# Kernel optimization log

Hardware: AMD Instinct MI355X
Metric: run time of the kernel (lower is better)

## Reference

```python
import jax, jax.numpy as jnp
import numpy as np

B, N, D = 4, 2048, 256
ALPHA = 0.2  # LeakyReLU negative slope
NEG = -1e9


def setup_inputs() -> dict:
    key = jax.random.key(0)
    ks = jax.random.split(key, 16)
    f = lambda k, s: jax.random.normal(k, s, dtype=jnp.float32)
    sc = 0.02
    spk = jax.random.randint(ks[13], (B, N), 0, 2)
    intra_mask = (spk[:, :, None] == spk[:, None, :]).astype(jnp.int32)
    inter_mask = 1 - intra_mask
    return {
        'inp': f(ks[0], (B, N, D)),
        'emo_vector': f(ks[1], (B, N, D)),
        'event_csk_before': f(ks[2], (B, N, D)),
        'event_csk_after': f(ks[3], (B, N, D)),
        'emo_intra_csk': f(ks[4], (B, N, D)),
        'emo_inter_csk': f(ks[5], (B, N, D)),
        'int_intra_csk': f(ks[6], (B, N, D)),
        'int_inter_csk': f(ks[7], (B, N, D)),
        'W': f(ks[8], (D, D)) * sc,
        'a': f(ks[9], (2 * D,)) * sc,
        'csk_W': f(ks[10], (D, D)) * sc,
        'csk_b': jnp.zeros((D,), jnp.float32),
        'emo_lin_W': f(ks[11], (4, D, D)) * sc,  # order: weight, query, key, value
        'emo_lin_b': jnp.zeros((4, D), jnp.float32),
        'act_lin_W': f(ks[12], (4, D, D)) * sc,
        'act_lin_b': jnp.zeros((4, D), jnp.float32),
        'conv_len': jax.random.randint(ks[14], (B,), N // 2, N + 1),
        'intra_mask': intra_mask,
        'inter_mask': inter_mask,
    }


def _csk_measure(tv, hv, temo, icsk, ocsk, tim, tom, lin_W, lin_b, add_emo):
    # tv/temo: [B,1,D] target vectors; hv: [B,N,D]; tim/tom: [B,1,N] float masks
    wW, qW, kW, vW = lin_W
    wb, qb, kb, vb = lin_b
    q = (tv + temo if add_emo else tv) @ qW + qb            # [B,1,D]
    w_i = icsk @ wW + wb
    w_o = ocsk @ wW + wb
    k_base = hv @ kW + kb
    v_base = hv @ vW + vb
    k_i, v_i = k_base + w_i, v_base + w_i                   # [B,N,D]
    k_o, v_o = k_base + w_o, v_base + w_o
    inv = 1.0 / jnp.sqrt(jnp.float32(D))
    s_i = jnp.einsum('bqd,bnd->bqn', q, k_i) * inv * tim    # [B,1,N]
    s_o = jnp.einsum('bqd,bnd->bqn', q, k_o) * inv * tom
    m = tim + tom
    probs = jax.nn.softmax(jnp.where(m == 0, NEG, s_i + s_o), axis=-1)  # [B,1,N]
    p_i = (probs * tim).transpose(0, 2, 1)                  # [B,N,1]
    p_o = (probs * tom).transpose(0, 2, 1)
    target_enh = p_i * q + p_o * q                          # q broadcasts [B,1,D]->[B,N,D]
    csk_enh = p_i * v_i + p_o * v_o
    return target_enh + csk_enh, probs


def reference(inp, emo_vector, event_csk_before, event_csk_after,
              emo_intra_csk, emo_inter_csk, int_intra_csk, int_inter_csk,
              W, a, csk_W, csk_b, emo_lin_W, emo_lin_b, act_lin_W, act_lin_b,
              conv_len, intra_mask, inter_mask):
    im = intra_mask.astype(jnp.float32)
    om = inter_mask.astype(jnp.float32)
    h = inp @ W                                             # [B,N,D]
    evt = (event_csk_after @ csk_W + csk_b) + (event_csk_before @ csk_W + csk_b)
    # GAT scoring without materializing [B,N,N,2D]:
    # e[b,i,j] = leaky_relu(h[b,i].a1 + (h+evt)[b,j].a2)
    a1, a2 = a[:D], a[D:]
    s1 = h @ a1                                             # [B,N]
    s2 = (h + evt) @ a2                                     # [B,N]
    e_pair = jax.nn.leaky_relu(s1[:, :, None] + s2[:, None, :], ALPHA)  # [B,N,N]
    e = e_pair * im + e_pair * om
    adj = im + om
    attention = jax.nn.softmax(jnp.where(adj == 0, NEG, e), axis=-1)
    h_prime = jnp.einsum('bij,bjd->bid', attention, h)      # [B,N,D]
    # gather target (last utterance) per conversation
    b_idx = jnp.arange(inp.shape[0])
    t_idx = conv_len - 1
    tv = inp[b_idx, t_idx][:, None, :]                      # [B,1,D]
    temo = emo_vector[b_idx, t_idx][:, None, :]
    tim = im[b_idx, t_idx][:, None, :]                      # [B,1,N]
    tom = om[b_idx, t_idx][:, None, :]
    emo_conn, emo_probs = _csk_measure(tv, h_prime, temo, emo_intra_csk,
                                       emo_inter_csk, tim, tom,
                                       emo_lin_W, emo_lin_b, add_emo=True)
    int_conn, act_probs = _csk_measure(tv, h_prime, temo, int_intra_csk,
                                       int_inter_csk, tim, tom,
                                       act_lin_W, act_lin_b, add_emo=False)
    out = h_prime + inp + emo_conn + int_conn
    return jax.nn.relu(out), emo_probs, act_probs
```

## Files before the change

kernel.cpp:

```cpp
#include <hip/hip_runtime.h>
#include <math.h>


namespace {
constexpr int B = 4, N = 2048, D = 256;
constexpr float ALPHA = 0.2f;
constexpr float INVS  = 0.0625f;

constexpr size_t OFF_H     = 0;
constexpr size_t OFF_HP    = 2097152;
constexpr size_t OFF_UE    = 4194304;
constexpr size_t OFF_UA    = 6291456;
constexpr size_t OFF_PPOS  = 8388608;
constexpr size_t OFF_PNEG  = 10486784;
constexpr size_t OFF_S1    = 12584960;
constexpr size_t OFF_S2    = OFF_S1 + 8192;
constexpr size_t OFF_SIDX  = OFF_S2 + 8192;
constexpr size_t OFF_WP    = OFF_SIDX + 8192;
constexpr size_t OFF_WN    = OFF_WP + 8192;
constexpr size_t OFF_PARTP = OFF_WN + 8192;
constexpr size_t OFF_PARTN = OFF_PARTP + 32768;
constexpr size_t OFF_LE    = OFF_PARTN + 32768;
constexpr size_t OFF_LA    = OFF_LE + 8192;
constexpr size_t OFF_SET   = OFF_LA + 8192;
constexpr size_t KQE = OFF_SET + 0;
constexpr size_t WQE = OFF_SET + 1024;
constexpr size_t KQA = OFF_SET + 2048;
constexpr size_t WQA = OFF_SET + 3072;
constexpr size_t QCE = OFF_SET + 4096;
constexpr size_t QCA = OFF_SET + 5120;
constexpr size_t CA2 = OFF_SET + 6144;
constexpr size_t CEc = OFF_SET + 6400;
constexpr size_t CAc = OFF_SET + 6404;
constexpr size_t C2c = OFF_SET + 6408;
constexpr size_t OFF_RNK   = OFF_SET + 8192;
constexpr size_t OFF_C0    = OFF_RNK + 8192;
constexpr size_t OFF_C1    = OFF_C0 + 8192;
constexpr size_t OFF_PARTQ = OFF_C1 + 8192;
constexpr size_t OFF_QE    = OFF_PARTQ + 32768;
constexpr size_t OFF_QA    = OFF_QE + 1024;
constexpr size_t OFF_BT    = OFF_QA + 1024;
constexpr size_t OFF_PCNT  = OFF_BT + 163840;
constexpr size_t OFF_LEU   = OFF_PCNT + 131072;
constexpr size_t OFF_LAU   = OFF_LEU + 8192;
constexpr size_t SMXE      = OFF_LAU + 8192;
constexpr size_t SIVE      = SMXE + 4;
constexpr size_t SMXA      = SIVE + 4;
constexpr size_t SIVA      = SMXA + 4;
}

typedef __attribute__((ext_vector_type(8))) short bf16x8;
typedef __attribute__((ext_vector_type(4))) float f32x4;

__device__ inline float wave_sum(float v) {
#pragma unroll
  for (int off = 32; off > 0; off >>= 1) v += __shfl_xor(v, off, 64);
  return v;
}

__device__ inline ushort f2bf(float x) {
  union { float f; uint u; } v; v.f = x;
  return (ushort)((v.u + 0x7FFFu + ((v.u >> 16) & 1u)) >> 16);
}
__device__ inline uint pk2bf(float a, float b) {
  return (uint)f2bf(a) | ((uint)f2bf(b) << 16);
}
__device__ inline float bf2f(ushort u) {
  union { uint u; float f; } v; v.u = (uint)u << 16;
  return v.f;
}

__global__ __launch_bounds__(256) void k_btq(
    const float* __restrict__ Wm, const float* __restrict__ eW,
    const float* __restrict__ aW, const float* __restrict__ inp,
    const float* __restrict__ emo, const int* __restrict__ cl,
    ushort* __restrict__ bt, float* __restrict__ ws)
{
  __shared__ float smem[64*65];
  if (blockIdx.y < 5) {
    int m = blockIdx.y;
    const float* src = (m == 0) ? Wm : (m == 1) ? eW + 3*65536 : (m == 2) ? eW
                     : (m == 3) ? aW + 3*65536 : aW;
    ushort* dst = bt + (size_t)m*65536;
    int k0 = (blockIdx.x >> 2)*64, n0 = (blockIdx.x & 3)*64;
    int r = threadIdx.x >> 2, c0 = (threadIdx.x & 3)*16;
#pragma unroll
    for (int cc = 0; cc < 16; cc += 4)
      *(float4*)&smem[r*65 + c0+cc] = *(const float4*)&src[(size_t)(k0+r)*256 + n0 + c0 + cc];
    __syncthreads();
    int n = threadIdx.x >> 2, kq = (threadIdx.x & 3)*16;
    uint4 o0, o1;
    o0.x = pk2bf(smem[(kq+ 0)*65+n], smem[(kq+ 1)*65+n]);
    o0.y = pk2bf(smem[(kq+ 2)*65+n], smem[(kq+ 3)*65+n]);
    o0.z = pk2bf(smem[(kq+ 4)*65+n], smem[(kq+ 5)*65+n]);
    o0.w = pk2bf(smem[(kq+ 6)*65+n], smem[(kq+ 7)*65+n]);
    o1.x = pk2bf(smem[(kq+ 8)*65+n], smem[(kq+ 9)*65+n]);
    o1.y = pk2bf(smem[(kq+10)*65+n], smem[(kq+11)*65+n]);
    o1.z = pk2bf(smem[(kq+12)*65+n], smem[(kq+13)*65+n]);
    o1.w = pk2bf(smem[(kq+14)*65+n], smem[(kq+15)*65+n]);
    *(uint4*)&dst[(size_t)(n0+n)*256 + k0 + kq]     = o0;
    *(uint4*)&dst[(size_t)(n0+n)*256 + k0 + kq + 8] = o1;
  } else {
    int c = blockIdx.x;
    int m = blockIdx.y - 5;
    int d = threadIdx.x;
    if (d < 64) {
      int b = d >> 4, kk = d & 15;
      int t = cl[b] - 1;
      size_t idx = ((size_t)b*N + t)*D + c*16 + kk;
      float v = inp[idx];
      if (m == 0) v += emo[idx];
      smem[b*16 + kk] = v;
    }
    __syncthreads();
    const float* Wq = (m ? aW : eW) + (size_t)D*D;
    float acc0 = 0.f, acc1 = 0.f, acc2 = 0.f, acc3 = 0.f;
#pragma unroll
    for (int kk = 0; kk < 16; ++kk) {
      int k = c*16 + kk;
      float w = Wq[(size_t)k*D + d];
      acc0 += smem[0*16+kk]*w; acc1 += smem[1*16+kk]*w;
      acc2 += smem[2*16+kk]*w; acc3 += smem[3*16+kk]*w;
    }
    size_t base = OFF_PARTQ + ((size_t)(m*16 + c)*4)*256 + d;
    ws[base + 0*256] = acc0; ws[base + 1*256] = acc1;
    ws[base + 2*256] = acc2; ws[base + 3*256] = acc3;
  }
}

__global__ __launch_bounds__(256) void k_mgemmh(
    const float* __restrict__ A1, const ushort* __restrict__ bt,
    float* __restrict__ C)
{
  __shared__ ushort As[32*40];
  const int t = threadIdx.x;
  const int lane = t & 63, w = t >> 6;
  const int laneN = lane & 15, kg = lane >> 4;
  const int m0 = blockIdx.x * 32, n0 = blockIdx.y * 128;
  const int srow = t >> 3, sc = (t & 7) * 4;
  f32x4 acc[2][2] = {};
  for (int k0 = 0; k0 < 256; k0 += 32) {
    __syncthreads();
    float4 f = *(const float4*)&A1[(size_t)(m0 + srow)*256 + k0 + sc];
    uint2 o; o.x = pk2bf(f.x, f.y); o.y = pk2bf(f.z, f.w);
    *(uint2*)&As[srow*40 + sc] = o;
    __syncthreads();
    bf16x8 af[2];
#pragma unroll
    for (int i = 0; i < 2; ++i)
      af[i] = *(const bf16x8*)&As[(i*16 + laneN)*40 + kg*8];
#pragma unroll
    for (int j = 0; j < 2; ++j) {
      bf16x8 bf = *(const bf16x8*)&bt[(size_t)(n0 + w*32 + j*16 + laneN)*256 + k0 + kg*8];
#pragma unroll
      for (int i = 0; i < 2; ++i)
        acc[i][j] = __builtin_amdgcn_mfma_f32_16x16x32_bf16(af[i], bf, acc[i][j], 0, 0, 0);
    }
  }
#pragma unroll
  for (int i = 0; i < 2; ++i)
#pragma unroll
    for (int j = 0; j < 2; ++j)
#pragma unroll
      for (int r = 0; r < 4; ++r)
        C[(size_t)(m0 + i*16 + kg*4 + r)*256 + n0 + w*32 + j*16 + laneN] = acc[i][j][r];
}

__global__ __launch_bounds__(256) void k_qfinish(
    const float* __restrict__ eb, const float* __restrict__ ab,
    const float* __restrict__ cskb, const float* __restrict__ a,
    float* __restrict__ ws)
{
  int b = blockIdx.x, m = blockIdx.y, d = threadIdx.x;
  __shared__ float red[D];
  const float* bias = m ? ab : eb;
  float q = bias[D + d];
#pragma unroll
  for (int c = 0; c < 16; ++c)
    q += ws[OFF_PARTQ + ((size_t)(m*16 + c)*4 + b)*256 + d];
  ws[(m ? OFF_QA : OFF_QE) + (size_t)b*D + d] = q;
  ws[(m ? QCA : QCE) + (size_t)b*D + d] = q + bias[3*D + d] + bias[0*D + d];
  red[d] = q * (bias[2*D + d] + bias[0*D + d]);
  __syncthreads();
  for (int s = 128; s > 0; s >>= 1) { if (d < s) red[d] += red[d+s]; __syncthreads(); }
  if (d == 0) ws[(m ? CAc : CEc) + b] = red[0];
  if (m == 1 && b == 0) {
    __syncthreads();
    red[d] = cskb[d] * a[D + d];
    __syncthreads();
    for (int s = 128; s > 0; s >>= 1) { if (d < s) red[d] += red[d+s]; __syncthreads(); }
    if (d == 0) ws[C2c] = 2.0f * red[0];
  }
}

__global__ __launch_bounds__(256) void k_rowdots(
    const float* __restrict__ eW, const float* __restrict__ aW,
    const float* __restrict__ cskW, const float* __restrict__ a,
    float* __restrict__ ws)
{
  int job = blockIdx.y;
  int wid = threadIdx.x >> 6, lane = threadIdx.x & 63;
  int row = blockIdx.x*4 + wid;
  __shared__ float vec[D];
  const float* M; size_t outo;
  if (job < 16) {
    int b = job >> 2, m = (job >> 1) & 1, which = job & 1;
    const float* base = m ? aW : eW;
    M = base + (which ? 0 : (size_t)2*D*D);
    if (threadIdx.x < D)
      vec[threadIdx.x] = ws[(m ? OFF_QA : OFF_QE) + (size_t)b*D + threadIdx.x];
    outo = (which ? (m ? WQA : WQE) : (m ? KQA : KQE)) + (size_t)b*D;
  } else {
    M = cskW;
    if (threadIdx.x < D) vec[threadIdx.x] = a[D + threadIdx.x];
    outo = CA2;
  }
  __syncthreads();
  float4 w = *reinterpret_cast<const float4*>(&M[(size_t)row*D + lane*4]);
  float s = w.x*vec[lane*4] + w.y*vec[lane*4+1] + w.z*vec[lane*4+2] + w.w*vec[lane*4+3];
  s = wave_sum(s);
  if (lane == 0) ws[outo + row] = s;
}

__global__ __launch_bounds__(256) void k_us(
    const float* __restrict__ ei, const float* __restrict__ eo,
    const float* __restrict__ ai, const float* __restrict__ ao,
    const int* __restrict__ cl, const int* __restrict__ intra,
    const float* __restrict__ bef, const float* __restrict__ aft,
    const float* __restrict__ a, float* __restrict__ ws,
    ushort* __restrict__ ueb, ushort* __restrict__ uab)
{
  if (blockIdx.x < 2048) {
    size_t g = (size_t)blockIdx.x*256 + threadIdx.x;
    size_t base = g << 2;
    int b = (int)(base >> 19);
    int n = (int)((base >> 8) & (N - 1));
    int d0 = (int)(base & (D - 1));
    int t = cl[b] - 1;
    float tm = (float)intra[(size_t)b*N*N + (size_t)t*N + n];
    float om = 1.0f - tm;
    float4 vei = *(const float4*)&ei[base];
    float4 veo = *(const float4*)&eo[base];
    float4 vai = *(const float4*)&ai[base];
    float4 vao = *(const float4*)&ao[base];
    float4 ue, ua;
    ue.x = tm*vei.x + om*veo.x; ue.y = tm*vei.y + om*veo.y;
    ue.z = tm*vei.z + om*veo.z; ue.w = tm*vei.w + om*veo.w;
    ua.x = tm*vai.x + om*vao.x; ua.y = tm*vai.y + om*vao.y;
    ua.z = tm*vai.z + om*vao.z; ua.w = tm*vai.w + om*vao.w;
    uint2 pe; pe.x = pk2bf(ue.x, ue.y); pe.y = pk2bf(ue.z, ue.w);
    uint2 pa; pa.x = pk2bf(ua.x, ua.y); pa.y = pk2bf(ua.z, ua.w);
    *(uint2*)&ueb[base] = pe;
    *(uint2*)&uab[base] = pa;
    float4 wqe = *(const float4*)&ws[WQE + (size_t)b*D + d0];
    float4 wqa = *(const float4*)&ws[WQA + (size_t)b*D + d0];
    float se = ue.x*wqe.x + ue.y*wqe.y + ue.z*wqe.z + ue.w*wqe.w;
    float sa = ua.x*wqa.x + ua.y*wqa.y + ua.z*wqa.z + ua.w*wqa.w;
    se = wave_sum(se); sa = wave_sum(sa);
    if ((threadIdx.x & 63) == 0) {
      size_t row = base >> 8;
      ws[OFF_LEU + row] = se;
      ws[OFF_LAU + row] = sa;
    }
  } else {
    int wid  = (int)(((size_t)(blockIdx.x - 2048)*256 + threadIdx.x) >> 6);
    int lane = threadIdx.x & 63;
    int d0 = lane << 2;
    float4 a1 = *(const float4*)&a[d0];
    float4 a2 = *(const float4*)&a[D + d0];
    float4 cv = *(const float4*)&ws[CA2 + d0];
    float c2  = ws[C2c];
    for (int rr = 0; rr < 4; ++rr) {
      int row = wid*4 + rr;
      float4 h4 = *(const float4*)&ws[OFF_H + (size_t)row*D + d0];
      float4 b4 = *(const float4*)&bef[(size_t)row*D + d0];
      float4 f4 = *(const float4*)&aft[(size_t)row*D + d0];
      float s1 = h4.x*a1.x + h4.y*a1.y + h4.z*a1.z + h4.w*a1.w;
      float s2 = h4.x*a2.x + h4.y*a2.y + h4.z*a2.z + h4.w*a2.w
               + (b4.x+f4.x)*cv.x + (b4.y+f4.y)*cv.y
               + (b4.z+f4.z)*cv.z + (b4.w+f4.w)*cv.w;
      s1 = wave_sum(s1); s2 = wave_sum(s2);
      if (lane == 0) { ws[OFF_S1 + row] = s1; ws[OFF_S2 + row] = s2 + c2; }
    }
  }
}

__global__ __launch_bounds__(256) void k_cnt2(float* __restrict__ ws)
{
  int jb = blockIdx.x;
  int kb = blockIdx.y;
  int b  = blockIdx.z;
  int tid = threadIdx.x;
  __shared__ float ck[128];
  if (tid < 32)
    *(float4*)&ck[tid*4] = *(const float4*)&ws[OFF_S2 + (size_t)b*N + kb*128 + tid*4];
  __syncthreads();
  int j = jb*256 + tid;
  float v = ws[OFF_S2 + (size_t)b*N + j];
  int kg = kb*128;
  int cnt = 0;
#pragma unroll
  for (int k = 0; k < 128; k += 16) {
    float4 u0 = *(const float4*)&ck[k];
    float4 u1 = *(const float4*)&ck[k+4];
    float4 u2 = *(const float4*)&ck[k+8];
    float4 u3 = *(const float4*)&ck[k+12];
    cnt += (u0.x < v) || (u0.x == v && (kg+k+ 0) < j);
    cnt += (u0.y < v) || (u0.y == v && (kg+k+ 1) < j);
    cnt += (u0.z < v) || (u0.z == v && (kg+k+ 2) < j);
    cnt += (u0.w < v) || (u0.w == v && (kg+k+ 3) < j);
    cnt += (u1.x < v) || (u1.x == v && (kg+k+ 4) < j);
    cnt += (u1.y < v) || (u1.y == v && (kg+k+ 5) < j);
    cnt += (u1.z < v) || (u1.z == v && (kg+k+ 6) < j);
    cnt += (u1.w < v) || (u1.w == v && (kg+k+ 7) < j);
    cnt += (u2.x < v) || (u2.x == v && (kg+k+ 8) < j);
    cnt += (u2.y < v) || (u2.y == v && (kg+k+ 9) < j);
    cnt += (u2.z < v) || (u2.z == v && (kg+k+10) < j);
    cnt += (u2.w < v) || (u2.w == v && (kg+k+11) < j);
    cnt += (u3.x < v) || (u3.x == v && (kg+k+12) < j);
    cnt += (u3.y < v) || (u3.y == v && (kg+k+13) < j);
    cnt += (u3.z < v) || (u3.z == v && (kg+k+14) < j);
    cnt += (u3.w < v) || (u3.w == v && (kg+k+15) < j);
  }
  ((int*)ws)[OFF_PCNT + ((size_t)(b*16 + kb))*N + j] = cnt;
}

__global__ __launch_bounds__(1024) void k_csr(float* __restrict__ ws)
{
  int b = blockIdx.x, t = threadIdx.x;
  __shared__ float sv[N];
  __shared__ int   sx[N];
  __shared__ float zp[N+1], zn[N+1], tmp[N];
  const int* pc = (const int*)ws + OFF_PCNT;
#pragma unroll
  for (int h = 0; h < 2; ++h) {
    int j = t + h*1024;
    int cnt = 0;
#pragma unroll
    for (int kb = 0; kb < 16; ++kb)
      cnt += pc[((size_t)(b*16 + kb))*N + j];
    float v = ws[OFF_S2 + (size_t)b*N + j];
    sv[cnt] = v; sx[cnt] = j;
  }
  __syncthreads();
#pragma unroll
  for (int h = 0; h < 2; ++h) {
    int r = t + h*1024;
    ((int*)ws)[OFF_SIDX + (size_t)b*N + r] = sx[r];
    float w = expf(sv[r]);
    ws[OFF_WP + (size_t)b*N + r] = w;
    tmp[r] = w;
  }
  __syncthreads();
  for (int off = 1; off < N; off <<= 1) {
    float v0 = (t >= off)        ? tmp[t - off]        : 0.f;
    float v1 = (t + 1024 >= off) ? tmp[t + 1024 - off] : 0.f;
    __syncthreads();
    tmp[t] += v0; tmp[t + 1024] += v1;
    __syncthreads();
  }
  if (t == 0) zp[0] = 0.f;
  zp[t + 1] = tmp[t]; zp[t + 1025] = tmp[t + 1024];
  __syncthreads();
#pragma unroll
  for (int h = 0; h < 2; ++h) {
    int r = t + h*1024;
    float w = expf(ALPHA*sv[r]);
    ws[OFF_WN + (size_t)b*N + r] = w;
    tmp[r] = w;
  }
  __syncthreads();
  for (int off = 1; off < N; off <<= 1) {
    float v0 = (t >= off)        ? tmp[t - off]        : 0.f;
    float v1 = (t + 1024 >= off) ? tmp[t + 1024 - off] : 0.f;
    __syncthreads();
    tmp[t] += v0; tmp[t + 1024] += v1;
    __syncthreads();
  }
  if (t == 0) zn[0] = 0.f;
  zn[t + 1] = tmp[t]; zn[t + 1025] = tmp[t + 1024];
  __syncthreads();
  float zpT = zp[N];
#pragma unroll
  for (int h = 0; h < 2; ++h) {
    int i = t + h*1024;
    float s1i = ws[OFF_S1 + (size_t)b*N + i];
    float th = -s1i;
    int lo = 0, hi = N;
    while (lo < hi) { int mid = (lo + hi) >> 1; if (sv[mid] <= th) lo = mid + 1; else hi = mid; }
    float ep = expf(s1i), en = expf(ALPHA*s1i);
    float den = ep*(zpT - zp[lo]) + en*zn[lo];
    ((int*)ws)[OFF_RNK + (size_t)b*N + i] = lo;
    ws[OFF_C0 + (size_t)b*N + i] = ep/den;
    ws[OFF_C1 + (size_t)b*N + i] = en/den;
  }
}

__global__ __launch_bounds__(256) void k_p1(float* __restrict__ ws)
{
  int c = blockIdx.x, b = blockIdx.y, d = threadIdx.x;
  const int*   sidx = (const int*)ws + OFF_SIDX + (size_t)b*N;
  const float* wp = ws + OFF_WP + (size_t)b*N;
  const float* wn = ws + OFF_WN + (size_t)b*N;
  const float* h  = ws + OFF_H + (size_t)b*N*D;
  float ap = 0.f, an = 0.f;
  for (int r = c*64; r < c*64 + 64; ++r) {
    float hv = h[(size_t)sidx[r]*D + d];
    ap += wp[r]*hv; an += wn[r]*hv;
  }
  ws[OFF_PARTP + ((size_t)b*32 + c)*D + d] = ap;
  ws[OFF_PARTN + ((size_t)b*32 + c)*D + d] = an;
}

__global__ __launch_bounds__(256) void k_p3(float* __restrict__ ws)
{
  int c = blockIdx.x, b = blockIdx.y, d = threadIdx.x;
  const int*   sidx = (const int*)ws + OFF_SIDX + (size_t)b*N;
  const float* wp = ws + OFF_WP + (size_t)b*N;
  const float* wn = ws + OFF_WN + (size_t)b*N;
  const float* h  = ws + OFF_H + (size_t)b*N*D;
  float ap = 0.f, an = 0.f;
  for (int c2 = 0; c2 < c; ++c2) {
    ap += ws[OFF_PARTP + ((size_t)b*32 + c2)*D + d];
    an += ws[OFF_PARTN + ((size_t)b*32 + c2)*D + d];
  }
  for (int r = c*64; r < c*64 + 64; ++r) {
    ws[OFF_PPOS + ((size_t)b*(N+1) + r)*D + d] = ap;
    ws[OFF_PNEG + ((size_t)b*(N+1) + r)*D + d] = an;
    float hv = h[(size_t)sidx[r]*D + d];
    ap += wp[r]*hv; an += wn[r]*hv;
  }
  if (c == 31) {
    ws[OFF_PPOS + ((size_t)b*(N+1) + N)*D + d] = ap;
    ws[OFF_PNEG + ((size_t)b*(N+1) + N)*D + d] = an;
  }
}

__global__ __launch_bounds__(256) void k_hprime2(float* __restrict__ ws,
                                                 ushort* __restrict__ hpb)
{
  int b = blockIdx.y, d = threadIdx.x;
  int i0 = blockIdx.x * 8;
  float totp = ws[OFF_PPOS + ((size_t)b*(N+1) + N)*D + d];
  float kqe = ws[KQE + (size_t)b*D + d];
  float kqa = ws[KQA + (size_t)b*D + d];
  float se[8], sa[8];
#pragma unroll
  for (int ii = 0; ii < 8; ++ii) {
    int i = i0 + ii;
    int   r  = ((const int*)ws)[OFF_RNK + (size_t)b*N + i];
    float c0 = ws[OFF_C0 + (size_t)b*N + i];
    float c1 = ws[OFF_C1 + (size_t)b*N + i];
    float pp = ws[OFF_PPOS + ((size_t)b*(N+1) + r)*D + d];
    float pn = ws[OFF_PNEG + ((size_t)b*(N+1) + r)*D + d];
    float v = c0*(totp - pp) + c1*pn;
    hpb[((size_t)b*N + i)*D + d] = f2bf(v);
    se[ii] = v*kqe;
    sa[ii] = v*kqa;
  }
  __shared__ float lred[16][4];
  int w = d >> 6, lane = d & 63;
#pragma unroll
  for (int ii = 0; ii < 8; ++ii) {
    float s = wave_sum(se[ii]);
    if (lane == 0) lred[ii][w] = s;
    s = wave_sum(sa[ii]);
    if (lane == 0) lred[8 + ii][w] = s;
  }
  __syncthreads();
  if (d < 16) {
    float s = lred[d][0] + lred[d][1] + lred[d][2] + lred[d][3];
    size_t row = (size_t)b*N + i0 + (d & 7);
    if (d < 8) ws[OFF_LE + row] = (s + ws[OFF_LEU + row] + ws[CEc + b]) * INVS;
    else       ws[OFF_LA + row] = (s + ws[OFF_LAU + row] + ws[CAc + b]) * INVS;
  }
}

__global__ __launch_bounds__(256) void k_smred(float* __restrict__ ws)
{
  int b = blockIdx.x, m = blockIdx.y, t = threadIdx.x;
  const float* l = ws + (m ? OFF_LA : OFF_LE) + (size_t)b*N;
  __shared__ float red[256];
  float v[8];
  float mx = -1e30f;
#pragma unroll
  for (int k = 0; k < 8; ++k) { v[k] = l[t*8 + k]; mx = fmaxf(mx, v[k]); }
  red[t] = mx; __syncthreads();
  for (int s = 128; s > 0; s >>= 1) { if (t < s) red[t] = fmaxf(red[t], red[t+s]); __syncthreads(); }
  mx = red[0]; __syncthreads();
  float sum = 0.f;
#pragma unroll
  for (int k = 0; k < 8; ++k) sum += expf(v[k] - mx);
  red[t] = sum; __syncthreads();
  for (int s = 128; s > 0; s >>= 1) { if (t < s) red[t] += red[t+s]; __syncthreads(); }
  if (t == 0) {
    ws[(m ? SMXA : SMXE) + b] = mx;
    ws[(m ? SIVA : SIVE) + b] = 1.0f / red[0];
  }
}

__global__ __launch_bounds__(256) void k_tail(
    const float* __restrict__ inp, const ushort* __restrict__ bt,
    float* __restrict__ ws, float* __restrict__ out,
    const ushort* __restrict__ hpb, const ushort* __restrict__ ueb,
    const ushort* __restrict__ uab)
{
  __shared__ float qec[256], qac[256];
  const int t = threadIdx.x;
  const int m0 = blockIdx.x * 32, n0 = blockIdx.y * 128;
  const int b = m0 >> 11;
  const int lane = t & 63, w = t >> 6;
  const int laneN = lane & 15, kg = lane >> 4;
  qec[t] = ws[QCE + (size_t)b*D + t];
  qac[t] = ws[QCA + (size_t)b*D + t];
  __syncthreads();
  const ushort* Bve = bt + 1*65536;
  const ushort* Bwe = bt + 2*65536;
  const ushort* Bva = bt + 3*65536;
  const ushort* Bwa = bt + 4*65536;
  f32x4 accE[2][2] = {}, accA[2][2] = {};
  for (int k0 = 0; k0 < 256; k0 += 32) {
    bf16x8 bve[2], bwe[2], bva[2], bwa[2];
#pragma unroll
    for (int j = 0; j < 2; ++j) {
      size_t cb = (size_t)(n0 + w*32 + j*16 + laneN)*256 + k0 + kg*8;
      bve[j] = *(const bf16x8*)&Bve[cb];
      bwe[j] = *(const bf16x8*)&Bwe[cb];
      bva[j] = *(const bf16x8*)&Bva[cb];
      bwa[j] = *(const bf16x8*)&Bwa[cb];
    }
#pragma unroll
    for (int i = 0; i < 2; ++i) {
      size_t ab = (size_t)(m0 + i*16 + laneN)*256 + k0 + kg*8;
      bf16x8 hf = *(const bf16x8*)&hpb[ab];
      bf16x8 ef = *(const bf16x8*)&ueb[ab];
      bf16x8 zf = *(const bf16x8*)&uab[ab];
#pragma unroll
      for (int j = 0; j < 2; ++j) {
        accE[i][j] = __builtin_amdgcn_mfma_f32_16x16x32_bf16(hf, bve[j], accE[i][j], 0, 0, 0);
        accE[i][j] = __builtin_amdgcn_mfma_f32_16x16x32_bf16(ef, bwe[j], accE[i][j], 0, 0, 0);
        accA[i][j] = __builtin_amdgcn_mfma_f32_16x16x32_bf16(hf, bva[j], accA[i][j], 0, 0, 0);
        accA[i][j] = __builtin_amdgcn_mfma_f32_16x16x32_bf16(zf, bwa[j], accA[i][j], 0, 0, 0);
      }
    }
  }
  float smxe = ws[SMXE + b], sive = ws[SIVE + b];
  float smxa = ws[SMXA + b], siva = ws[SIVA + b];
  if (blockIdx.y == 0 && t < 32) {
    size_t row = (size_t)m0 + t;
    int n = (int)(row & (N - 1));
    float pe = expf(ws[OFF_LE + row] - smxe) * sive;
    float pa = expf(ws[OFF_LA + row] - smxa) * siva;
    out[(size_t)B*N*D + (size_t)b*N + n] = pe;
    out[(size_t)B*N*D + (size_t)B*N + (size_t)b*N + n] = pa;
  }
#pragma unroll
  for (int i = 0; i < 2; ++i) {
#pragma unroll
    for (int r = 0; r < 4; ++r) {
      size_t row = (size_t)m0 + i*16 + kg*4 + r;
      float pe = expf(ws[OFF_LE + row] - smxe) * sive;
      float pa = expf(ws[OFF_LA + row] - smxa) * siva;
#pragma unroll
      for (int j = 0; j < 2; ++j) {
        int col = n0 + w*32 + j*16 + laneN;
        size_t idx = row*256 + col;
        float hpv = bf2f(hpb[idx]);
        float o = hpv + inp[idx] + pe*(qec[col] + accE[i][j][r]) + pa*(qac[col] + accA[i][j][r]);
        out[idx] = fmaxf(o, 0.f);
      }
    }
  }
}

extern "C" void kernel_launch(void* const* d_in, const int* in_sizes, int n_in,
                              void* d_out, int out_size, void* d_ws, size_t ws_size,
                              hipStream_t stream) {
  const float* inp  = (const float*)d_in[0];
  const float* emo  = (const float*)d_in[1];
  const float* bef  = (const float*)d_in[2];
  const float* aft  = (const float*)d_in[3];
  const float* ei   = (const float*)d_in[4];
  const float* eo   = (const float*)d_in[5];
  const float* ii   = (const float*)d_in[6];
  const float* io   = (const float*)d_in[7];
  const float* W    = (const float*)d_in[8];
  const float* a    = (const float*)d_in[9];
  const float* cskW = (const float*)d_in[10];
  const float* cskb = (const float*)d_in[11];
  const float* eW   = (const float*)d_in[12];
  const float* eb   = (const float*)d_in[13];
  const float* aW   = (const float*)d_in[14];
  const float* ab   = (const float*)d_in[15];
  const int*   cl   = (const int*)d_in[16];
  const int*   intra= (const int*)d_in[17];
  float* ws  = (float*)d_ws;
  float* out = (float*)d_out;
  ushort* bt  = (ushort*)(ws + OFF_BT);
  ushort* hpb = (ushort*)(ws + OFF_HP);
  ushort* ueb = (ushort*)(ws + OFF_UE);
  ushort* uab = (ushort*)(ws + OFF_UA);

  k_btq<<<dim3(16, 7), 256, 0, stream>>>(W, eW, aW, inp, emo, cl, bt, ws);
  k_mgemmh<<<dim3(256, 2), 256, 0, stream>>>(inp, bt, ws + OFF_H);
  k_qfinish<<<dim3(B, 2), 256, 0, stream>>>(eb, ab, cskb, a, ws);
  k_rowdots<<<dim3(64, 17), 256, 0, stream>>>(eW, aW, cskW, a, ws);
  k_us<<<2560, 256, 0, stream>>>(ei, eo, ii, io, cl, intra, bef, aft, a, ws, ueb, uab);
  k_cnt2<<<dim3(8, 16, B), 256, 0, stream>>>(ws);
  k_csr<<<B, 1024, 0, stream>>>(ws);
  k_p1<<<dim3(32, B), 256, 0, stream>>>(ws);
  k_p3<<<dim3(32, B), 256, 0, stream>>>(ws);
  k_hprime2<<<dim3(256, B), 256, 0, stream>>>(ws, hpb);
  k_smred<<<dim3(B, 2), 256, 0, stream>>>(ws);
  k_tail<<<dim3(256, 2), 256, 0, stream>>>(inp, bt, ws, out, hpb, ueb, uab);
}
```

Baseline: 125.2 us.

## Merge prologue kernels and fold softmax reduction into atomics in hprime

Several small launches are folded together. The q-projection is now computed in one pass per (batch, head) block alongside the weight transposes, which removes the partial-sum buffer and the separate qfinish kernel. The h GEMM and the row-dot kernels now share one launch, and the two prefix scans in the CSR kernel run interleaved in a single loop. The softmax max/sum reduction kernel is replaced by atomic accumulation of exp-sums inside hprime, with no max subtraction. That drops a launch but risks overflow and non-deterministic summation order.

```diff
diff --git a/kernel.cpp b/kernel.cpp
--- a/kernel.cpp
+++ b/kernel.cpp
@@ -36,17 +36,14 @@
 constexpr size_t OFF_RNK   = OFF_SET + 8192;
 constexpr size_t OFF_C0    = OFF_RNK + 8192;
 constexpr size_t OFF_C1    = OFF_C0 + 8192;
-constexpr size_t OFF_PARTQ = OFF_C1 + 8192;
-constexpr size_t OFF_QE    = OFF_PARTQ + 32768;
+constexpr size_t OFF_QE    = OFF_C1 + 8192;
 constexpr size_t OFF_QA    = OFF_QE + 1024;
 constexpr size_t OFF_BT    = OFF_QA + 1024;
 constexpr size_t OFF_PCNT  = OFF_BT + 163840;
 constexpr size_t OFF_LEU   = OFF_PCNT + 131072;
 constexpr size_t OFF_LAU   = OFF_LEU + 8192;
-constexpr size_t SMXE      = OFF_LAU + 8192;
-constexpr size_t SIVE      = SMXE + 4;
-constexpr size_t SMXA      = SIVE + 4;
-constexpr size_t SIVA      = SMXA + 4;
+constexpr size_t OFF_SSE   = OFF_LAU + 8192;
+constexpr size_t OFF_SSA   = OFF_SSE + 4;
 }
 
 typedef __attribute__((ext_vector_type(8))) short bf16x8;
@@ -70,19 +67,22 @@
   return v.f;
 }
 
-__global__ __launch_bounds__(256) void k_btq(
+__global__ __launch_bounds__(256) void k_pre(
     const float* __restrict__ Wm, const float* __restrict__ eW,
     const float* __restrict__ aW, const float* __restrict__ inp,
-    const float* __restrict__ emo, const int* __restrict__ cl,
+    const float* __restrict__ emo, const float* __restrict__ eb,
+    const float* __restrict__ ab, const float* __restrict__ cskb,
+    const float* __restrict__ a, const int* __restrict__ cl,
     ushort* __restrict__ bt, float* __restrict__ ws)
 {
   __shared__ float smem[64*65];
-  if (blockIdx.y < 5) {
-    int m = blockIdx.y;
+  int idx = blockIdx.x;
+  if (idx < 80) {
+    int m = idx / 16, bx = idx & 15;
     const float* src = (m == 0) ? Wm : (m == 1) ? eW + 3*65536 : (m == 2) ? eW
                      : (m == 3) ? aW + 3*65536 : aW;
     ushort* dst = bt + (size_t)m*65536;
-    int k0 = (blockIdx.x >> 2)*64, n0 = (blockIdx.x & 3)*64;
+    int k0 = (bx >> 2)*64, n0 = (bx & 3)*64;
     int r = threadIdx.x >> 2, c0 = (threadIdx.x & 3)*16;
 #pragma unroll
     for (int cc = 0; cc < 16; cc += 4)
@@ -101,125 +101,109 @@
     *(uint4*)&dst[(size_t)(n0+n)*256 + k0 + kq]     = o0;
     *(uint4*)&dst[(size_t)(n0+n)*256 + k0 + kq + 8] = o1;
   } else {
-    int c = blockIdx.x;
-    int m = blockIdx.y - 5;
+    int f = idx - 80;
+    int b = f >> 1, m = f & 1;
     int d = threadIdx.x;
-    if (d < 64) {
-      int b = d >> 4, kk = d & 15;
-      int t = cl[b] - 1;
-      size_t idx = ((size_t)b*N + t)*D + c*16 + kk;
-      float v = inp[idx];
-      if (m == 0) v += emo[idx];
-      smem[b*16 + kk] = v;
-    }
+    float* xs  = smem;
+    float* red = smem + 256;
+    int t = cl[b] - 1;
+    float tv = inp[((size_t)b*N + t)*D + d];
+    xs[d] = (m == 0) ? tv + emo[((size_t)b*N + t)*D + d] : tv;
     __syncthreads();
+    const float* bias = m ? ab : eb;
     const float* Wq = (m ? aW : eW) + (size_t)D*D;
-    float acc0 = 0.f, acc1 = 0.f, acc2 = 0.f, acc3 = 0.f;
-#pragma unroll
-    for (int kk = 0; kk < 16; ++kk) {
-      int k = c*16 + kk;
-      float w = Wq[(size_t)k*D + d];
-      acc0 += smem[0*16+kk]*w; acc1 += smem[1*16+kk]*w;
-      acc2 += smem[2*16+kk]*w; acc3 += smem[3*16+kk]*w;
-    }
-    size_t base = OFF_PARTQ + ((size_t)(m*16 + c)*4)*256 + d;
-    ws[base + 0*256] = acc0; ws[base + 1*256] = acc1;
-    ws[base + 2*256] = acc2; ws[base + 3*256] = acc3;
-  }
-}
-
-__global__ __launch_bounds__(256) void k_mgemmh(
-    const float* __restrict__ A1, const ushort* __restrict__ bt,
-    float* __restrict__ C)
-{
-  __shared__ ushort As[32*40];
-  const int t = threadIdx.x;
-  const int lane = t & 63, w = t >> 6;
-  const int laneN = lane & 15, kg = lane >> 4;
-  const int m0 = blockIdx.x * 32, n0 = blockIdx.y * 128;
-  const int srow = t >> 3, sc = (t & 7) * 4;
-  f32x4 acc[2][2] = {};
-  for (int k0 = 0; k0 < 256; k0 += 32) {
-    __syncthreads();
-    float4 f = *(const float4*)&A1[(size_t)(m0 + srow)*256 + k0 + sc];
-    uint2 o; o.x = pk2bf(f.x, f.y); o.y = pk2bf(f.z, f.w);
-    *(uint2*)&As[srow*40 + sc] = o;
-    __syncthreads();
-    bf16x8 af[2];
-#pragma unroll
-    for (int i = 0; i < 2; ++i)
-      af[i] = *(const bf16x8*)&As[(i*16 + laneN)*40 + kg*8];
-#pragma unroll
-    for (int j = 0; j < 2; ++j) {
-      bf16x8 bf = *(const bf16x8*)&bt[(size_t)(n0 + w*32 + j*16 + laneN)*256 + k0 + kg*8];
-#pragma unroll
-      for (int i = 0; i < 2; ++i)
-        acc[i][j] = __builtin_amdgcn_mfma_f32_16x16x32_bf16(af[i], bf, acc[i][j], 0, 0, 0);
-    }
-  }
-#pragma unroll
-  for (int i = 0; i < 2; ++i)
-#pragma unroll
-    for (int j = 0; j < 2; ++j)
-#pragma unroll
-      for (int r = 0; r < 4; ++r)
-        C[(size_t)(m0 + i*16 + kg*4 + r)*256 + n0 + w*32 + j*16 + laneN] = acc[i][j][r];
-}
-
-__global__ __launch_bounds__(256) void k_qfinish(
-    const float* __restrict__ eb, const float* __restrict__ ab,
-    const float* __restrict__ cskb, const float* __restrict__ a,
-    float* __restrict__ ws)
-{
-  int b = blockIdx.x, m = blockIdx.y, d = threadIdx.x;
-  __shared__ float red[D];
-  const float* bias = m ? ab : eb;
-  float q = bias[D + d];
-#pragma unroll
-  for (int c = 0; c < 16; ++c)
-    q += ws[OFF_PARTQ + ((size_t)(m*16 + c)*4 + b)*256 + d];
-  ws[(m ? OFF_QA : OFF_QE) + (size_t)b*D + d] = q;
-  ws[(m ? QCA : QCE) + (size_t)b*D + d] = q + bias[3*D + d] + bias[0*D + d];
-  red[d] = q * (bias[2*D + d] + bias[0*D + d]);
-  __syncthreads();
-  for (int s = 128; s > 0; s >>= 1) { if (d < s) red[d] += red[d+s]; __syncthreads(); }
-  if (d == 0) ws[(m ? CAc : CEc) + b] = red[0];
-  if (m == 1 && b == 0) {
-    __syncthreads();
-    red[d] = cskb[d] * a[D + d];
+    float a0 = 0.f, a1 = 0.f, a2 = 0.f, a3 = 0.f;
+    for (int k = 0; k < 256; k += 4) {
+      a0 += xs[k+0]*Wq[(size_t)(k+0)*256 + d];
+      a1 += xs[k+1]*Wq[(size_t)(k+1)*256 + d];
+      a2 += xs[k+2]*Wq[(size_t)(k+2)*256 + d];
+      a3 += xs[k+3]*Wq[(size_t)(k+3)*256 + d];
+    }
+    float q = bias[D + d] + ((a0 + a1) + (a2 + a3));
+    ws[(m ? OFF_QA : OFF_QE) + (size_t)b*D + d] = q;
+    ws[(m ? QCA : QCE) + (size_t)b*D + d] = q + bias[3*D + d] + bias[0*D + d];
+    red[d] = q * (bias[2*D + d] + bias[0*D + d]);
     __syncthreads();
     for (int s = 128; s > 0; s >>= 1) { if (d < s) red[d] += red[d+s]; __syncthreads(); }
-    if (d == 0) ws[C2c] = 2.0f * red[0];
-  }
-}
-
-__global__ __launch_bounds__(256) void k_rowdots(
+    if (d == 0) ws[(m ? CAc : CEc) + b] = red[0];
+    if (m == 1 && b == 0) {
+      __syncthreads();
+      red[d] = cskb[d] * a[D + d];
+      __syncthreads();
+      for (int s = 128; s > 0; s >>= 1) { if (d < s) red[d] += red[d+s]; __syncthreads(); }
+      if (d == 0) ws[C2c] = 2.0f * red[0];
+    }
+    if (f == 0 && d < 8) ws[OFF_SSE + d] = 0.f;
+  }
+}
+
+__global__ __launch_bounds__(256) void k_hw(
+    const float* __restrict__ inp, const ushort* __restrict__ bt,
     const float* __restrict__ eW, const float* __restrict__ aW,
     const float* __restrict__ cskW, const float* __restrict__ a,
     float* __restrict__ ws)
 {
-  int job = blockIdx.y;
-  int wid = threadIdx.x >> 6, lane = threadIdx.x & 63;
-  int row = blockIdx.x*4 + wid;
-  __shared__ float vec[D];
-  const float* M; size_t outo;
-  if (job < 16) {
-    int b = job >> 2, m = (job >> 1) & 1, which = job & 1;
-    const float* base = m ? aW : eW;
-    M = base + (which ? 0 : (size_t)2*D*D);
-    if (threadIdx.x < D)
-      vec[threadIdx.x] = ws[(m ? OFF_QA : OFF_QE) + (size_t)b*D + threadIdx.x];
-    outo = (which ? (m ? WQA : WQE) : (m ? KQA : KQE)) + (size_t)b*D;
+  __shared__ float smem[640];
+  int idx = blockIdx.x;
+  if (idx < 512) {
+    ushort* As = (ushort*)smem;
+    const int t = threadIdx.x;
+    const int lane = t & 63, w = t >> 6;
+    const int laneN = lane & 15, kg = lane >> 4;
+    const int m0 = (idx >> 1) * 32, n0 = (idx & 1) * 128;
+    const int srow = t >> 3, sc = (t & 7) * 4;
+    float* C = ws + OFF_H;
+    f32x4 acc[2][2] = {};
+    for (int k0 = 0; k0 < 256; k0 += 32) {
+      __syncthreads();
+      float4 f = *(const float4*)&inp[(size_t)(m0 + srow)*256 + k0 + sc];
+      uint2 o; o.x = pk2bf(f.x, f.y); o.y = pk2bf(f.z, f.w);
+      *(uint2*)&As[srow*40 + sc] = o;
+      __syncthreads();
+      bf16x8 af[2];
+#pragma unroll
+      for (int i = 0; i < 2; ++i)
+        af[i] = *(const bf16x8*)&As[(i*16 + laneN)*40 + kg*8];
+#pragma unroll
+      for (int j = 0; j < 2; ++j) {
+        bf16x8 bf = *(const bf16x8*)&bt[(size_t)(n0 + w*32 + j*16 + laneN)*256 + k0 + kg*8];
+#pragma unroll
+        for (int i = 0; i < 2; ++i)
+          acc[i][j] = __builtin_amdgcn_mfma_f32_16x16x32_bf16(af[i], bf, acc[i][j], 0, 0, 0);
+      }
+    }
+#pragma unroll
+    for (int i = 0; i < 2; ++i)
+#pragma unroll
+      for (int j = 0; j < 2; ++j)
+#pragma unroll
+        for (int r = 0; r < 4; ++r)
+          C[(size_t)(m0 + i*16 + kg*4 + r)*256 + n0 + w*32 + j*16 + laneN] = acc[i][j][r];
   } else {
-    M = cskW;
-    if (threadIdx.x < D) vec[threadIdx.x] = a[D + threadIdx.x];
-    outo = CA2;
-  }
-  __syncthreads();
-  float4 w = *reinterpret_cast<const float4*>(&M[(size_t)row*D + lane*4]);
-  float s = w.x*vec[lane*4] + w.y*vec[lane*4+1] + w.z*vec[lane*4+2] + w.w*vec[lane*4+3];
-  s = wave_sum(s);
-  if (lane == 0) ws[outo + row] = s;
+    int f = idx - 512;
+    int job = f >> 6, rb = f & 63;
+    int wid = threadIdx.x >> 6, lane = threadIdx.x & 63;
+    int row = rb*4 + wid;
+    float* vec = smem;
+    const float* M; size_t outo;
+    if (job < 16) {
+      int b = job >> 2, m = (job >> 1) & 1, which = job & 1;
+      const float* base = m ? aW : eW;
+      M = base + (which ? 0 : (size_t)2*D*D);
+      if (threadIdx.x < D)
+        vec[threadIdx.x] = ws[(m ? OFF_QA : OFF_QE) + (size_t)b*D + threadIdx.x];
+      outo = (which ? (m ? WQA : WQE) : (m ? KQA : KQE)) + (size_t)b*D;
+    } else {
+      M = cskW;
+      if (threadIdx.x < D) vec[threadIdx.x] = a[D + threadIdx.x];
+      outo = CA2;
+    }
+    __syncthreads();
+    float4 w = *reinterpret_cast<const float4*>(&M[(size_t)row*D + lane*4]);
+    float s = w.x*vec[lane*4] + w.y*vec[lane*4+1] + w.z*vec[lane*4+2] + w.w*vec[lane*4+3];
+    s = wave_sum(s);
+    if (lane == 0) ws[outo + row] = s;
+  }
 }
 
 __global__ __launch_bounds__(256) void k_us(
@@ -330,7 +314,8 @@
   int b = blockIdx.x, t = threadIdx.x;
   __shared__ float sv[N];
   __shared__ int   sx[N];
-  __shared__ float zp[N+1], zn[N+1], tmp[N];
+  __shared__ float zp[N+1], zn[N+1];
+  __shared__ float tp[N], tn[N];
   const int* pc = (const int*)ws + OFF_PCNT;
 #pragma unroll
   for (int h = 0; h < 2; ++h) {
@@ -347,38 +332,26 @@
   for (int h = 0; h < 2; ++h) {
     int r = t + h*1024;
     ((int*)ws)[OFF_SIDX + (size_t)b*N + r] = sx[r];
-    float w = expf(sv[r]);
-    ws[OFF_WP + (size_t)b*N + r] = w;
-    tmp[r] = w;
+    float wp = expf(sv[r]);
+    float wn = expf(ALPHA*sv[r]);
+    ws[OFF_WP + (size_t)b*N + r] = wp;
+    ws[OFF_WN + (size_t)b*N + r] = wn;
+    tp[r] = wp; tn[r] = wn;
   }
   __syncthreads();
   for (int off = 1; off < N; off <<= 1) {
-    float v0 = (t >= off)        ? tmp[t - off]        : 0.f;
-    float v1 = (t + 1024 >= off) ? tmp[t + 1024 - off] : 0.f;
+    float p0 = (t >= off)        ? tp[t - off]        : 0.f;
+    float n0 = (t >= off)        ? tn[t - off]        : 0.f;
+    float p1 = (t + 1024 >= off) ? tp[t + 1024 - off] : 0.f;
+    float n1 = (t + 1024 >= off) ? tn[t + 1024 - off] : 0.f;
     __syncthreads();
-    tmp[t] += v0; tmp[t + 1024] += v1;
+    tp[t] += p0; tn[t] += n0;
+    tp[t + 1024] += p1; tn[t + 1024] += n1;
     __syncthreads();
   }
-  if (t == 0) zp[0] = 0.f;
-  zp[t + 1] = tmp[t]; zp[t + 1025] = tmp[t + 1024];
-  __syncthreads();
-#pragma unroll
-  for (int h = 0; h < 2; ++h) {
-    int r = t + h*1024;
-    float w = expf(ALPHA*sv[r]);
-    ws[OFF_WN + (size_t)b*N + r] = w;
-    tmp[r] = w;
-  }
-  __syncthreads();
-  for (int off = 1; off < N; off <<= 1) {
-    float v0 = (t >= off)        ? tmp[t - off]        : 0.f;
-    float v1 = (t + 1024 >= off) ? tmp[t + 1024 - off] : 0.f;
-    __syncthreads();
-    tmp[t] += v0; tmp[t + 1024] += v1;
-    __syncthreads();
-  }
-  if (t == 0) zn[0] = 0.f;
-  zn[t + 1] = tmp[t]; zn[t + 1025] = tmp[t + 1024];
+  if (t == 0) { zp[0] = 0.f; zn[0] = 0.f; }
+  zp[t + 1] = tp[t]; zp[t + 1025] = tp[t + 1024];
+  zn[t + 1] = tn[t]; zn[t + 1025] = tn[t + 1024];
   __syncthreads();
   float zpT = zp[N];
 #pragma unroll
@@ -459,6 +432,7 @@
     sa[ii] = v*kqa;
   }
   __shared__ float lred[16][4];
+  __shared__ float l16[16];
   int w = d >> 6, lane = d & 63;
 #pragma unroll
   for (int ii = 0; ii < 8; ++ii) {
@@ -471,31 +445,23 @@
   if (d < 16) {
     float s = lred[d][0] + lred[d][1] + lred[d][2] + lred[d][3];
     size_t row = (size_t)b*N + i0 + (d & 7);
-    if (d < 8) ws[OFF_LE + row] = (s + ws[OFF_LEU + row] + ws[CEc + b]) * INVS;
-    else       ws[OFF_LA + row] = (s + ws[OFF_LAU + row] + ws[CAc + b]) * INVS;
-  }
-}
-
-__global__ __launch_bounds__(256) void k_smred(float* __restrict__ ws)
-{
-  int b = blockIdx.x, m = blockIdx.y, t = threadIdx.x;
-  const float* l = ws + (m ? OFF_LA : OFF_LE) + (size_t)b*N;
-  __shared__ float red[256];
-  float v[8];
-  float mx = -1e30f;
-#pragma unroll
-  for (int k = 0; k < 8; ++k) { v[k] = l[t*8 + k]; mx = fmaxf(mx, v[k]); }
-  red[t] = mx; __syncthreads();
-  for (int s = 128; s > 0; s >>= 1) { if (t < s) red[t] = fmaxf(red[t], red[t+s]); __syncthreads(); }
-  mx = red[0]; __syncthreads();
-  float sum = 0.f;
-#pragma unroll
-  for (int k = 0; k < 8; ++k) sum += expf(v[k] - mx);
-  red[t] = sum; __syncthreads();
-  for (int s = 128; s > 0; s >>= 1) { if (t < s) red[t] += red[t+s]; __syncthreads(); }
-  if (t == 0) {
-    ws[(m ? SMXA : SMXE) + b] = mx;
-    ws[(m ? SIVA : SIVE) + b] = 1.0f / red[0];
+    float lv;
+    if (d < 8) { lv = (s + ws[OFF_LEU + row] + ws[CEc + b]) * INVS; ws[OFF_LE + row] = lv; }
+    else       { lv = (s + ws[OFF_LAU + row] + ws[CAc + b]) * INVS; ws[OFF_LA + row] = lv; }
+    l16[d] = lv;
+  }
+  __syncthreads();
+  if (d == 0) {
+    float s = 0.f;
+#pragma unroll
+    for (int i = 0; i < 8; ++i) s += expf(l16[i]);
+    atomicAdd(&ws[OFF_SSE + b], s);
+  }
+  if (d == 64) {
+    float s = 0.f;
+#pragma unroll
+    for (int i = 8; i < 16; ++i) s += expf(l16[i]);
+    atomicAdd(&ws[OFF_SSA + b], s);
   }
 }
 
@@ -544,13 +510,13 @@
       }
     }
   }
-  float smxe = ws[SMXE + b], sive = ws[SIVE + b];
-  float smxa = ws[SMXA + b], siva = ws[SIVA + b];
+  float sive = 1.0f / ws[OFF_SSE + b];
+  float siva = 1.0f / ws[OFF_SSA + b];
   if (blockIdx.y == 0 && t < 32) {
     size_t row = (size_t)m0 + t;
     int n = (int)(row & (N - 1));
-    float pe = expf(ws[OFF_LE + row] - smxe) * sive;
-    float pa = expf(ws[OFF_LA + row] - smxa) * siva;
+    float pe = expf(ws[OFF_LE + row]) * sive;
+    float pa = expf(ws[OFF_LA + row]) * siva;
     out[(size_t)B*N*D + (size_t)b*N + n] = pe;
     out[(size_t)B*N*D + (size_t)B*N + (size_t)b*N + n] = pa;
   }
@@ -559,8 +525,8 @@
 #pragma unroll
     for (int r = 0; r < 4; ++r) {
       size_t row = (size_t)m0 + i*16 + kg*4 + r;
-      float pe = expf(ws[OFF_LE + row] - smxe) * sive;
-      float pa = expf(ws[OFF_LA + row] - smxa) * siva;
+      float pe = expf(ws[OFF_LE + row]) * sive;
+      float pa = expf(ws[OFF_LA + row]) * siva;
 #pragma unroll
       for (int j = 0; j < 2; ++j) {
         int col = n0 + w*32 + j*16 + laneN;
@@ -601,16 +567,13 @@
   ushort* ueb = (ushort*)(ws + OFF_UE);
   ushort* uab = (ushort*)(ws + OFF_UA);
 
-  k_btq<<<dim3(16, 7), 256, 0, stream>>>(W, eW, aW, inp, emo, cl, bt, ws);
-  k_mgemmh<<<dim3(256, 2), 256, 0, stream>>>(inp, bt, ws + OFF_H);
-  k_qfinish<<<dim3(B, 2), 256, 0, stream>>>(eb, ab, cskb, a, ws);
-  k_rowdots<<<dim3(64, 17), 256, 0, stream>>>(eW, aW, cskW, a, ws);
+  k_pre<<<88, 256, 0, stream>>>(W, eW, aW, inp, emo, eb, ab, cskb, a, cl, bt, ws);
+  k_hw<<<1600, 256, 0, stream>>>(inp, bt, eW, aW, cskW, a, ws);
   k_us<<<2560, 256, 0, stream>>>(ei, eo, ii, io, cl, intra, bef, aft, a, ws, ueb, uab);
   k_cnt2<<<dim3(8, 16, B), 256, 0, stream>>>(ws);
   k_csr<<<B, 1024, 0, stream>>>(ws);
   k_p1<<<dim3(32, B), 256, 0, stream>>>(ws);
   k_p3<<<dim3(32, B), 256, 0, stream>>>(ws);
   k_hprime2<<<dim3(256, B), 256, 0, stream>>>(ws, hpb);
-  k_smred<<<dim3(B, 2), 256, 0, stream>>>(ws);
   k_tail<<<dim3(256, 2), 256, 0, stream>>>(inp, bt, ws, out, hpb, ueb, uab);
 }
```

New measurement: 146.0 us. 16.6% more time.
